# Optimization experiments

Measured on AMD Instinct MI355X. Metric: run time of the kernel, lower is better.

Reference implementation:

```python
import jax, jax.numpy as jnp
import numpy as np

# Bayer pattern 'gbrg': 2x2 channel map (0=R,1=G,2=B)
#   (0,0)=G (0,1)=B
#   (1,0)=R (1,1)=G
CMAP = np.array([[1, 2], [0, 1]], dtype=np.int32)
XP = np.linspace(0.0, 255.0, 17).astype(np.float32)  # LUT knots

# 3x3 Gaussian blur kernel, sigma=0.4 (torchvision GaussianBlur)
def _gauss_kernel(sigma=0.4):
    x = np.array([-1.0, 0.0, 1.0], dtype=np.float32)
    g = np.exp(-(x ** 2) / (2.0 * sigma ** 2))
    g /= g.sum()
    return (g[:, None] * g[None, :]).astype(np.float32)

BLUR_K = _gauss_kernel()[None, None]  # [1,1,3,3]

# Malvar-He-Cutler demosaic kernels (/8)
_G_AT = np.array([[0,0,-1,0,0],[0,0,2,0,0],[-1,2,4,2,-1],[0,0,2,0,0],[0,0,-1,0,0]], np.float32) / 8.0
_K_H = np.array([[0,0,0.5,0,0],[0,-1,0,-1,0],[-1,4,5,4,-1],[0,-1,0,-1,0],[0,0,0.5,0,0]], np.float32) / 8.0
_K_V = _K_H.T.copy()
_K_D = np.array([[0,0,-1.5,0,0],[0,2,0,2,0],[-1.5,0,6,0,-1.5],[0,2,0,2,0],[0,0,-1.5,0,0]], np.float32) / 8.0
DEMOSAIC_K = np.stack([_G_AT, _K_H, _K_V, _K_D])[:, None]  # [4,1,5,5]


def _conv_reflect(x, k):
    p = k.shape[-1] // 2
    xp_ = jnp.pad(x, ((0, 0), (0, 0), (p, p), (p, p)), mode='reflect')
    return jax.lax.conv_general_dilated(xp_, jnp.asarray(k), (1, 1), 'VALID',
                                        dimension_numbers=('NCHW', 'OIHW', 'NCHW'))


def setup_inputs() -> dict:
    key = jax.random.key(0)
    k1, k2, k3, k4 = jax.random.split(key, 4)
    B, H, W = 32, 512, 512
    im = jax.random.uniform(k1, (B, 3, H, W), jnp.float32)           # normalized RGB
    yp = jnp.sort(jax.random.uniform(k2, (3, 17), jnp.float32) * 255.0, axis=1)  # per-channel calib curves
    sigma = 10.0 + 2.0 * jax.random.normal(k3, ())                   # N(noise_sigma, 2) draw
    noise = sigma * jax.random.normal(k4, (B, 1, H, W), jnp.float32)
    return {"im": im, "yp": yp, "noise": noise}


def reference(im, yp, noise):
    B, _, H, W = im.shape
    ys = jnp.arange(H) % 2
    xs = jnp.arange(W) % 2
    cmap = jnp.asarray(CMAP)[ys[:, None], xs[None, :]]               # [H,W] channel at each pixel

    im255 = im * 255.0
    # Mosaic: pick bayer channel at each pixel -> [B,1,H,W]
    bayer = jnp.take_along_axis(im255, cmap[None, None], axis=1)

    # Gaussian blur (reflect padding)
    blurred = _conv_reflect(bayer, BLUR_K)

    # Per-bayer-channel piecewise-linear calibration (np.interp semantics)
    xp_knots = jnp.asarray(XP)
    lin_r = jnp.interp(blurred, xp_knots, yp[0])
    lin_g = jnp.interp(blurred, xp_knots, yp[1])
    lin_b = jnp.interp(blurred, xp_knots, yp[2])
    c = cmap[None, None]
    linear = jnp.where(c == 0, lin_r, jnp.where(c == 1, lin_g, lin_b))

    # Additive noise
    noisy = linear + noise

    # Malvar demosaic: one 4-filter conv, then per-position selection
    f = _conv_reflect(noisy, DEMOSAIC_K)                             # [B,4,H,W]
    g_f, h_f, v_f, d_f = f[:, 0], f[:, 1], f[:, 2], f[:, 3]
    raw = noisy[:, 0]
    my = ys[:, None]
    mx = xs[None, :]
    p00 = (my == 0) & (mx == 0)   # G (blue row, red col)
    p01 = (my == 0) & (mx == 1)   # B
    p10 = (my == 1) & (mx == 0)   # R
    p11 = (my == 1) & (mx == 1)   # G (red row, blue col)

    R = jnp.where(p10, raw, jnp.where(p11, h_f, jnp.where(p00, v_f, d_f)))
    G = jnp.where(p00 | p11, raw, g_f)
    Bc = jnp.where(p01, raw, jnp.where(p00, h_f, jnp.where(p11, v_f, d_f)))
    rgb = jnp.stack([R, G, Bc], axis=1)                              # [B,3,H,W]

    return jnp.clip(rgb / 255.0, 0.0, 1.0)
```

## Files before the change

### kernel.cpp

```cpp
#include <hip/hip_runtime.h>


#define TDS 16

typedef float f4u __attribute__((ext_vector_type(4), aligned(16)));

struct HB { float hb0, hb1, hb2, hb3, hh0, hh1; };
struct MR { f4u a, b, ae, be; };
struct NZ { f4u z; float ze0, ze1; };

__device__ __forceinline__ int refl(int i, int n) {
    return i < 0 ? -i : (i >= n ? 2 * n - 2 - i : i);
}

__device__ __forceinline__ float clip01(float x) {
    return fminf(fmaxf(x * (1.0f / 255.0f), 0.0f), 1.0f);
}

__global__ __launch_bounds__(256, 2) void camera_kernel(
    const float* __restrict__ im, const float* __restrict__ yp,
    const float* __restrict__ noise, float* __restrict__ out,
    int H, int W)
{
    __shared__ float2 s_tab[4][48];

    const int tid  = threadIdx.x;
    const int wv   = tid >> 6;
    const int lane = tid & 63;
    const int b    = blockIdx.z;

    const int stripes = W >> 8;
    const int slot    = blockIdx.x * 4 + wv;
    const int stripe  = slot % stripes;
    const int gy0     = (slot / stripes) * TDS;
    const int gx0     = stripe << 8;
    const int x0      = gx0 + 4 * lane;

    const size_t HW = (size_t)H * W;
    const float* p0  = im + (size_t)b * 3 * HW;
    const float* p1  = p0 + HW;
    const float* nzb = noise + (size_t)b * HW;

    if (lane < 48) {
        int ch = lane >> 4, i = lane & 15;
        s_tab[wv][lane] = make_float2(yp[ch * 17 + i], yp[ch * 17 + i + 1]);
    }
    asm volatile("s_waitcnt lgkmcnt(0)" ::: "memory");
    const float2* tabw = s_tab[wv];

    const bool l0   = (lane == 0), l63 = (lane == 63);
    const bool lInt = l0  && (gx0 != 0);
    const bool rInt = l63 && (x0 + 4 != W);
    const bool eInt = lInt || rInt;
    const bool eAny = l0 || l63;
    const int  xe   = l0 ? x0 - 4 : x0 + 4;
    const int  xen  = l0 ? x0 - 2 : x0 + 4;

    const float g0 = 0.04038794f;
    const float g1 = 0.91922413f;

    auto itp = [&](float tv, int ch) -> float {
        float s = tv * 16.0f;
        int i = (int)s; i = i < 0 ? 0 : (i > 15 ? 15 : i);
        float2 p = tabw[ch * 16 + i];
        return fmaf(s - (float)i, p.y - p.x, p.x);
    };

    auto ldmos = [&](int t) -> MR {
        MR m;
        int yr = refl(t, H);
        const float* pe = (t & 1) ? p0 : p1;
        const float* re = pe + (size_t)yr * W;
        const float* ro = re + HW;
        m.a = *(const f4u*)(re + x0);
        m.b = *(const f4u*)(ro + x0);
        m.ae = m.a; m.be = m.b;
        if (eInt) {
            m.ae = *(const f4u*)(re + xe);
            m.be = *(const f4u*)(ro + xe);
        }
        return m;
    };
    auto ldnz = [&](int t) -> NZ {
        NZ z;
        int yr = refl(t, H);
        const float* nzr = nzb + (size_t)yr * W;
        z.z = *(const f4u*)(nzr + x0);
        z.ze0 = 0.f; z.ze1 = 0.f;
        if (eInt) {
            float2 e = *(const float2*)(nzr + xen);
            z.ze0 = e.x; z.ze1 = e.y;
        }
        return z;
    };

    auto hblur = [&](const MR& q) -> HB {
        float m0 = q.a.x, m1 = q.b.y, m2 = q.a.z, m3 = q.b.w;
        float ml = __shfl_up(m3, 1, 64);
        float mr = __shfl_down(m0, 1, 64);
        float me0 = q.ae.x, me1 = q.be.y, me2 = q.ae.z, me3 = q.be.w;
        if (l0)  ml = lInt ? me3 : m1;
        if (l63) mr = rInt ? me0 : m2;
        HB h;
        h.hb0 = fmaf(g0, ml + m1, g1 * m0);
        h.hb1 = fmaf(g0, m0 + m2, g1 * m1);
        h.hb2 = fmaf(g0, m1 + m3, g1 * m2);
        h.hb3 = fmaf(g0, m2 + mr, g1 * m3);
        float hL0 = fmaf(g0, me1 + me3, g1 * me2);
        float hL1 = fmaf(g0, me2 + m0,  g1 * me3);
        float hR0 = fmaf(g0, m3 + me1,  g1 * me0);
        float hR1 = fmaf(g0, me0 + me2, g1 * me1);
        h.hh0 = l0 ? hL0 : hR0;
        h.hh1 = l0 ? hL1 : hR1;
        return h;
    };

    float ring[5][8];
    HB hA = hblur(ldmos(gy0 - 3));
    HB hB = hblur(ldmos(gy0 - 2));
    MR mN = ldmos(gy0 - 1);
    NZ zN = ldnz(gy0 - 2);
    const size_t outb = (size_t)b * 3 * HW;

    #pragma unroll
    for (int k = 0; k < TDS + 4; ++k) {
        const int r = gy0 - 2 + k;
        MR mC = mN;
        NZ zC = zN;
        if (k < TDS + 3) {
            mN = ldmos(r + 2);
            zN = ldnz(r + 1);
        }
        HB hC = hblur(mC);
        float tb0 = fmaf(g0, hA.hb0 + hC.hb0, g1 * hB.hb0);
        float tb1 = fmaf(g0, hA.hb1 + hC.hb1, g1 * hB.hb1);
        float tb2 = fmaf(g0, hA.hb2 + hC.hb2, g1 * hB.hb2);
        float tb3 = fmaf(g0, hA.hb3 + hC.hb3, g1 * hB.hb3);
        float th0 = fmaf(g0, hA.hh0 + hC.hh0, g1 * hB.hh0);
        float th1 = fmaf(g0, hA.hh1 + hC.hh1, g1 * hB.hh1);
        const int chE = (k & 1) ? 0 : 1;
        const int chO = chE + 1;
        float c0 = itp(tb0, chE) + zC.z.x;
        float c1 = itp(tb1, chO) + zC.z.y;
        float c2 = itp(tb2, chE) + zC.z.z;
        float c3 = itp(tb3, chO) + zC.z.w;
        float e0 = 0.f, e1 = 0.f;
        if (eAny) { e0 = itp(th0, chE) + zC.ze0; e1 = itp(th1, chO) + zC.ze1; }
        float hl0 = __shfl_up(c2, 1, 64);
        float hl1 = __shfl_up(c3, 1, 64);
        float hr0 = __shfl_down(c0, 1, 64);
        float hr1 = __shfl_down(c1, 1, 64);
        if (l0)  { hl0 = lInt ? e0 : c2;  hl1 = lInt ? e1 : c1; }
        if (l63) { hr0 = rInt ? e0 : c2;  hr1 = rInt ? e1 : c1; }
        ring[k % 5][0] = hl0; ring[k % 5][1] = hl1;
        ring[k % 5][2] = c0;  ring[k % 5][3] = c1;
        ring[k % 5][4] = c2;  ring[k % 5][5] = c3;
        ring[k % 5][6] = hr0; ring[k % 5][7] = hr1;
        hA = hB; hB = hC;

        if (k >= 4) {
            const int y = gy0 + k - 4;
            float Rv[4], Gv[4], Bv[4];
            #pragma unroll
            for (int j = 0; j < 4; ++j) {
                const int cj = 2 + j;
                float c    = ring[(k - 2) % 5][cj];
                float ax1x = ring[(k - 2) % 5][cj - 1] + ring[(k - 2) % 5][cj + 1];
                float ax2x = ring[(k - 2) % 5][cj - 2] + ring[(k - 2) % 5][cj + 2];
                float ax1y = ring[(k - 3) % 5][cj] + ring[(k - 1) % 5][cj];
                float diag = ring[(k - 3) % 5][cj - 1] + ring[(k - 3) % 5][cj + 1]
                           + ring[(k - 1) % 5][cj - 1] + ring[(k - 1) % 5][cj + 1];
                float ax2y = ring[(k - 4) % 5][cj] + ring[k % 5][cj];
                const bool xO = (j & 1) != 0;
                const bool yO = (k & 1) != 0;
                float R, G, Bc;
                if (!yO && !xO) {
                    float hh = (0.5f * ax2y - diag - ax2x + 4.f * ax1x + 5.f * c) * 0.125f;
                    float vv = (0.5f * ax2x - diag - ax2y + 4.f * ax1y + 5.f * c) * 0.125f;
                    R = vv; G = c; Bc = hh;
                } else if (!yO && xO) {
                    float gg = (2.f * (ax1y + ax1x) - ax2y - ax2x + 4.f * c) * 0.125f;
                    float dd = (2.f * diag - 1.5f * (ax2y + ax2x) + 6.f * c) * 0.125f;
                    R = dd; G = gg; Bc = c;
                } else if (yO && !xO) {
                    float gg = (2.f * (ax1y + ax1x) - ax2y - ax2x + 4.f * c) * 0.125f;
                    float dd = (2.f * diag - 1.5f * (ax2y + ax2x) + 6.f * c) * 0.125f;
                    R = c; G = gg; Bc = dd;
                } else {
                    float hh = (0.5f * ax2y - diag - ax2x + 4.f * ax1x + 5.f * c) * 0.125f;
                    float vv = (0.5f * ax2x - diag - ax2y + 4.f * ax1y + 5.f * c) * 0.125f;
                    R = hh; G = c; Bc = vv;
                }
                Rv[j] = clip01(R); Gv[j] = clip01(G); Bv[j] = clip01(Bc);
            }
            size_t o = outb + (size_t)y * W + x0;
            *(f4u*)(out + o)          = (f4u){Rv[0], Rv[1], Rv[2], Rv[3]};
            *(f4u*)(out + o + HW)     = (f4u){Gv[0], Gv[1], Gv[2], Gv[3]};
            *(f4u*)(out + o + 2 * HW) = (f4u){Bv[0], Bv[1], Bv[2], Bv[3]};
        }
    }
}

extern "C" void kernel_launch(void* const* d_in, const int* in_sizes, int n_in,
                              void* d_out, int out_size, void* d_ws, size_t ws_size,
                              hipStream_t stream) {
    const float* im    = (const float*)d_in[0];
    const float* yp    = (const float*)d_in[1];
    const float* noise = (const float*)d_in[2];
    float* out = (float*)d_out;

    const int H = 512, W = 512;
    const int B = in_sizes[2] / (H * W);

    const int stripes = W / 256;
    const int slots   = stripes * (H / TDS);
    dim3 grid(slots / 4, 1, B);
    camera_kernel<<<grid, 256, 0, stream>>>(im, yp, noise, out, H, W);
}
```

Baseline: 40.88 us.

## Narrow per-lane width from four to two pixels, doubling wave count

Each lane now handles 2 columns instead of 4, so a wave covers a 128-wide stripe and the grid launches twice as many blocks. Loads and stores become 8-byte vectors, the ring buffer shrinks, and the blur, interpolation and demosaic logic are rewritten for the narrower footprint, including new edge-lane handling. The aim is more parallelism and lower register pressure for better latency hiding on a memory-bound kernel. In exchange, each wave does more redundant halo loads and more shuffles per pixel, and the narrower accesses are less efficient.

After: 40.48 us. No clear change (-1.0%).

```diff
diff --git a/kernel.cpp b/kernel.cpp
--- a/kernel.cpp
+++ b/kernel.cpp
@@ -3,11 +3,12 @@
 
 #define TDS 16
 
+typedef float f2u __attribute__((ext_vector_type(2), aligned(8)));
 typedef float f4u __attribute__((ext_vector_type(4), aligned(16)));
 
-struct HB { float hb0, hb1, hb2, hb3, hh0, hh1; };
-struct MR { f4u a, b, ae, be; };
-struct NZ { f4u z; float ze0, ze1; };
+struct HB { float hb0, hb1, hh0, hh1; };
+struct MR { f2u a, b; f4u ae, be; };
+struct NZ { f2u z; float ze0, ze1; };
 
 __device__ __forceinline__ int refl(int i, int n) {
     return i < 0 ? -i : (i >= n ? 2 * n - 2 - i : i);
@@ -29,12 +30,12 @@
     const int lane = tid & 63;
     const int b    = blockIdx.z;
 
-    const int stripes = W >> 8;
+    const int stripes = W >> 7;
     const int slot    = blockIdx.x * 4 + wv;
     const int stripe  = slot % stripes;
     const int gy0     = (slot / stripes) * TDS;
-    const int gx0     = stripe << 8;
-    const int x0      = gx0 + 4 * lane;
+    const int gx0     = stripe << 7;
+    const int x0      = gx0 + 2 * lane;
 
     const size_t HW = (size_t)H * W;
     const float* p0  = im + (size_t)b * 3 * HW;
@@ -50,11 +51,10 @@
 
     const bool l0   = (lane == 0), l63 = (lane == 63);
     const bool lInt = l0  && (gx0 != 0);
-    const bool rInt = l63 && (x0 + 4 != W);
+    const bool rInt = l63 && (x0 + 2 != W);
     const bool eInt = lInt || rInt;
-    const bool eAny = l0 || l63;
-    const int  xe   = l0 ? x0 - 4 : x0 + 4;
-    const int  xen  = l0 ? x0 - 2 : x0 + 4;
+    const int  xe   = l0 ? x0 - 4 : x0 + 2;
+    const int  xen  = l0 ? x0 - 2 : x0 + 2;
 
     const float g0 = 0.04038794f;
     const float g1 = 0.91922413f;
@@ -72,9 +72,10 @@
         const float* pe = (t & 1) ? p0 : p1;
         const float* re = pe + (size_t)yr * W;
         const float* ro = re + HW;
-        m.a = *(const f4u*)(re + x0);
-        m.b = *(const f4u*)(ro + x0);
-        m.ae = m.a; m.be = m.b;
+        m.a = *(const f2u*)(re + x0);
+        m.b = *(const f2u*)(ro + x0);
+        m.ae = (f4u){0.f, 0.f, 0.f, 0.f};
+        m.be = (f4u){0.f, 0.f, 0.f, 0.f};
         if (eInt) {
             m.ae = *(const f4u*)(re + xe);
             m.be = *(const f4u*)(ro + xe);
@@ -85,7 +86,7 @@
         NZ z;
         int yr = refl(t, H);
         const float* nzr = nzb + (size_t)yr * W;
-        z.z = *(const f4u*)(nzr + x0);
+        z.z = *(const f2u*)(nzr + x0);
         z.ze0 = 0.f; z.ze1 = 0.f;
         if (eInt) {
             float2 e = *(const float2*)(nzr + xen);
@@ -95,27 +96,84 @@
     };
 
     auto hblur = [&](const MR& q) -> HB {
-        float m0 = q.a.x, m1 = q.b.y, m2 = q.a.z, m3 = q.b.w;
-        float ml = __shfl_up(m3, 1, 64);
+        float m0 = q.a.x, m1 = q.b.y;
+        float ml = __shfl_up(m1, 1, 64);
         float mr = __shfl_down(m0, 1, 64);
         float me0 = q.ae.x, me1 = q.be.y, me2 = q.ae.z, me3 = q.be.w;
         if (l0)  ml = lInt ? me3 : m1;
-        if (l63) mr = rInt ? me0 : m2;
+        if (l63) mr = rInt ? me0 : m0;
         HB h;
         h.hb0 = fmaf(g0, ml + m1, g1 * m0);
-        h.hb1 = fmaf(g0, m0 + m2, g1 * m1);
-        h.hb2 = fmaf(g0, m1 + m3, g1 * m2);
-        h.hb3 = fmaf(g0, m2 + mr, g1 * m3);
+        h.hb1 = fmaf(g0, m0 + mr, g1 * m1);
         float hL0 = fmaf(g0, me1 + me3, g1 * me2);
         float hL1 = fmaf(g0, me2 + m0,  g1 * me3);
-        float hR0 = fmaf(g0, m3 + me1,  g1 * me0);
+        float hR0 = fmaf(g0, m1 + me1,  g1 * me0);
         float hR1 = fmaf(g0, me0 + me2, g1 * me1);
         h.hh0 = l0 ? hL0 : hR0;
         h.hh1 = l0 ? hL1 : hR1;
         return h;
     };
 
-    float ring[5][8];
+    auto mknoisy = [&](const HB& a, const HB& bq, const HB& c,
+                       const NZ& z, int chE, float* rg) {
+        float tb0 = fmaf(g0, a.hb0 + c.hb0, g1 * bq.hb0);
+        float tb1 = fmaf(g0, a.hb1 + c.hb1, g1 * bq.hb1);
+        float th0 = fmaf(g0, a.hh0 + c.hh0, g1 * bq.hh0);
+        float th1 = fmaf(g0, a.hh1 + c.hh1, g1 * bq.hh1);
+        const int chO = chE + 1;
+        float c0 = itp(tb0, chE) + z.z.x;
+        float c1 = itp(tb1, chO) + z.z.y;
+        float e0 = 0.f, e1 = 0.f;
+        if (eInt) {
+            e0 = itp(th0, chE) + z.ze0;
+            e1 = itp(th1, chO) + z.ze1;
+        }
+        float hl0 = __shfl_up(c0, 1, 64);
+        float hl1 = __shfl_up(c1, 1, 64);
+        float hr0 = __shfl_down(c0, 1, 64);
+        float hr1 = __shfl_down(c1, 1, 64);
+        if (l0)  { hl0 = lInt ? e0 : hr0;  hl1 = lInt ? e1 : c1; }
+        if (l63) { hr0 = rInt ? e0 : c0;   hr1 = rInt ? e1 : hl1; }
+        rg[0] = hl0; rg[1] = hl1; rg[2] = c0;
+        rg[3] = c1;  rg[4] = hr0; rg[5] = hr1;
+    };
+
+    auto dem = [&](const float* u2, const float* u1, const float* ct,
+                   const float* d1, const float* d2, bool yO,
+                   float* Rv, float* Gv, float* Bv) {
+        #pragma unroll
+        for (int j = 0; j < 2; ++j) {
+            const int cj = 2 + j;
+            float c    = ct[cj];
+            float ax1x = ct[cj - 1] + ct[cj + 1];
+            float ax2x = ct[cj - 2] + ct[cj + 2];
+            float ax1y = u1[cj] + d1[cj];
+            float diag = u1[cj - 1] + u1[cj + 1] + d1[cj - 1] + d1[cj + 1];
+            float ax2y = u2[cj] + d2[cj];
+            const bool xO = (j & 1) != 0;
+            float R, G, Bc;
+            if (!yO && !xO) {
+                float hh = (0.5f * ax2y - diag - ax2x + 4.f * ax1x + 5.f * c) * 0.125f;
+                float vv = (0.5f * ax2x - diag - ax2y + 4.f * ax1y + 5.f * c) * 0.125f;
+                R = vv; G = c; Bc = hh;
+            } else if (!yO && xO) {
+                float gg = (2.f * (ax1y + ax1x) - ax2y - ax2x + 4.f * c) * 0.125f;
+                float dd = (2.f * diag - 1.5f * (ax2y + ax2x) + 6.f * c) * 0.125f;
+                R = dd; G = gg; Bc = c;
+            } else if (yO && !xO) {
+                float gg = (2.f * (ax1y + ax1x) - ax2y - ax2x + 4.f * c) * 0.125f;
+                float dd = (2.f * diag - 1.5f * (ax2y + ax2x) + 6.f * c) * 0.125f;
+                R = c; G = gg; Bc = dd;
+            } else {
+                float hh = (0.5f * ax2y - diag - ax2x + 4.f * ax1x + 5.f * c) * 0.125f;
+                float vv = (0.5f * ax2x - diag - ax2y + 4.f * ax1y + 5.f * c) * 0.125f;
+                R = hh; G = c; Bc = vv;
+            }
+            Rv[j] = clip01(R); Gv[j] = clip01(G); Bv[j] = clip01(Bc);
+        }
+    };
+
+    float ring[5][6];
     HB hA = hblur(ldmos(gy0 - 3));
     HB hB = hblur(ldmos(gy0 - 2));
     MR mN = ldmos(gy0 - 1);
@@ -132,71 +190,19 @@
             zN = ldnz(r + 1);
         }
         HB hC = hblur(mC);
-        float tb0 = fmaf(g0, hA.hb0 + hC.hb0, g1 * hB.hb0);
-        float tb1 = fmaf(g0, hA.hb1 + hC.hb1, g1 * hB.hb1);
-        float tb2 = fmaf(g0, hA.hb2 + hC.hb2, g1 * hB.hb2);
-        float tb3 = fmaf(g0, hA.hb3 + hC.hb3, g1 * hB.hb3);
-        float th0 = fmaf(g0, hA.hh0 + hC.hh0, g1 * hB.hh0);
-        float th1 = fmaf(g0, hA.hh1 + hC.hh1, g1 * hB.hh1);
         const int chE = (k & 1) ? 0 : 1;
-        const int chO = chE + 1;
-        float c0 = itp(tb0, chE) + zC.z.x;
-        float c1 = itp(tb1, chO) + zC.z.y;
-        float c2 = itp(tb2, chE) + zC.z.z;
-        float c3 = itp(tb3, chO) + zC.z.w;
-        float e0 = 0.f, e1 = 0.f;
-        if (eAny) { e0 = itp(th0, chE) + zC.ze0; e1 = itp(th1, chO) + zC.ze1; }
-        float hl0 = __shfl_up(c2, 1, 64);
-        float hl1 = __shfl_up(c3, 1, 64);
-        float hr0 = __shfl_down(c0, 1, 64);
-        float hr1 = __shfl_down(c1, 1, 64);
-        if (l0)  { hl0 = lInt ? e0 : c2;  hl1 = lInt ? e1 : c1; }
-        if (l63) { hr0 = rInt ? e0 : c2;  hr1 = rInt ? e1 : c1; }
-        ring[k % 5][0] = hl0; ring[k % 5][1] = hl1;
-        ring[k % 5][2] = c0;  ring[k % 5][3] = c1;
-        ring[k % 5][4] = c2;  ring[k % 5][5] = c3;
-        ring[k % 5][6] = hr0; ring[k % 5][7] = hr1;
+        mknoisy(hA, hB, hC, zC, chE, ring[k % 5]);
         hA = hB; hB = hC;
 
         if (k >= 4) {
             const int y = gy0 + k - 4;
-            float Rv[4], Gv[4], Bv[4];
-            #pragma unroll
-            for (int j = 0; j < 4; ++j) {
-                const int cj = 2 + j;
-                float c    = ring[(k - 2) % 5][cj];
-                float ax1x = ring[(k - 2) % 5][cj - 1] + ring[(k - 2) % 5][cj + 1];
-                float ax2x = ring[(k - 2) % 5][cj - 2] + ring[(k - 2) % 5][cj + 2];
-                float ax1y = ring[(k - 3) % 5][cj] + ring[(k - 1) % 5][cj];
-                float diag = ring[(k - 3) % 5][cj - 1] + ring[(k - 3) % 5][cj + 1]
-                           + ring[(k - 1) % 5][cj - 1] + ring[(k - 1) % 5][cj + 1];
-                float ax2y = ring[(k - 4) % 5][cj] + ring[k % 5][cj];
-                const bool xO = (j & 1) != 0;
-                const bool yO = (k & 1) != 0;
-                float R, G, Bc;
-                if (!yO && !xO) {
-                    float hh = (0.5f * ax2y - diag - ax2x + 4.f * ax1x + 5.f * c) * 0.125f;
-                    float vv = (0.5f * ax2x - diag - ax2y + 4.f * ax1y + 5.f * c) * 0.125f;
-                    R = vv; G = c; Bc = hh;
-                } else if (!yO && xO) {
-                    float gg = (2.f * (ax1y + ax1x) - ax2y - ax2x + 4.f * c) * 0.125f;
-                    float dd = (2.f * diag - 1.5f * (ax2y + ax2x) + 6.f * c) * 0.125f;
-                    R = dd; G = gg; Bc = c;
-                } else if (yO && !xO) {
-                    float gg = (2.f * (ax1y + ax1x) - ax2y - ax2x + 4.f * c) * 0.125f;
-                    float dd = (2.f * diag - 1.5f * (ax2y + ax2x) + 6.f * c) * 0.125f;
-                    R = c; G = gg; Bc = dd;
-                } else {
-                    float hh = (0.5f * ax2y - diag - ax2x + 4.f * ax1x + 5.f * c) * 0.125f;
-                    float vv = (0.5f * ax2x - diag - ax2y + 4.f * ax1y + 5.f * c) * 0.125f;
-                    R = hh; G = c; Bc = vv;
-                }
-                Rv[j] = clip01(R); Gv[j] = clip01(G); Bv[j] = clip01(Bc);
-            }
+            float Rv[2], Gv[2], Bv[2];
+            dem(ring[(k - 4) % 5], ring[(k - 3) % 5], ring[(k - 2) % 5],
+                ring[(k - 1) % 5], ring[k % 5], (k & 1) != 0, Rv, Gv, Bv);
             size_t o = outb + (size_t)y * W + x0;
-            *(f4u*)(out + o)          = (f4u){Rv[0], Rv[1], Rv[2], Rv[3]};
-            *(f4u*)(out + o + HW)     = (f4u){Gv[0], Gv[1], Gv[2], Gv[3]};
-            *(f4u*)(out + o + 2 * HW) = (f4u){Bv[0], Bv[1], Bv[2], Bv[3]};
+            *(f2u*)(out + o)          = (f2u){Rv[0], Rv[1]};
+            *(f2u*)(out + o + HW)     = (f2u){Gv[0], Gv[1]};
+            *(f2u*)(out + o + 2 * HW) = (f2u){Bv[0], Bv[1]};
         }
     }
 }
@@ -212,7 +218,7 @@
     const int H = 512, W = 512;
     const int B = in_sizes[2] / (H * W);
 
-    const int stripes = W / 256;
+    const int stripes = W / 128;
     const int slots   = stripes * (H / TDS);
     dim3 grid(slots / 4, 1, B);
     camera_kernel<<<grid, 256, 0, stream>>>(im, yp, noise, out, H, W);
```
